# Kernel tuning notes

Hardware: AMD Instinct MI355X
Metric: run time of the kernel (lower is better)

## Reference

```python
import jax, jax.numpy as jnp
import numpy as np

D, H, F, L, V = 768, 4, 1024, 3, 10000
B, TLAB, S = 16, 513, 197
SCALE = 0.02


def setup_inputs() -> dict:
    key = jax.random.key(0)
    ks = jax.random.split(key, 16)
    inp = {
        'labels': jax.random.randint(ks[0], (B, TLAB), 0, V),
        'vision_feats': jax.random.normal(ks[1], (B, S, D), jnp.float32),
        'vis_proj_w': jax.random.normal(ks[2], (D, D), jnp.float32) * SCALE,
        'vis_proj_b': jnp.zeros((D,), jnp.float32),
        'tok_emb': jax.random.normal(ks[3], (V, D), jnp.float32) * SCALE,
        'pos_emb': jax.random.normal(ks[4], (1, 512, D), jnp.float32) * SCALE,
        'sa_w': jax.random.normal(ks[5], (L, 3 * D, D), jnp.float32) * SCALE,
        'sa_b': jnp.zeros((L, 3 * D), jnp.float32),
        'sa_out_w': jax.random.normal(ks[6], (L, D, D), jnp.float32) * SCALE,
        'sa_out_b': jnp.zeros((L, D), jnp.float32),
        'ca_w': jax.random.normal(ks[7], (L, 3 * D, D), jnp.float32) * SCALE,
        'ca_b': jnp.zeros((L, 3 * D), jnp.float32),
        'ca_out_w': jax.random.normal(ks[8], (L, D, D), jnp.float32) * SCALE,
        'ca_out_b': jnp.zeros((L, D), jnp.float32),
        'ln1_g': jnp.ones((L, D), jnp.float32), 'ln1_b': jnp.zeros((L, D), jnp.float32),
        'ln2_g': jnp.ones((L, D), jnp.float32), 'ln2_b': jnp.zeros((L, D), jnp.float32),
        'ln3_g': jnp.ones((L, D), jnp.float32), 'ln3_b': jnp.zeros((L, D), jnp.float32),
        'ff1_w': jax.random.normal(ks[9], (L, F, D), jnp.float32) * SCALE,
        'ff1_b': jnp.zeros((L, F), jnp.float32),
        'ff2_w': jax.random.normal(ks[10], (L, D, F), jnp.float32) * SCALE,
        'ff2_b': jnp.zeros((L, D), jnp.float32),
        'out_w': jax.random.normal(ks[11], (V, D), jnp.float32) * SCALE,
        'out_b': jnp.zeros((V,), jnp.float32),
    }
    return inp


def layer_norm(x, g, b, eps=1e-5):
    m = jnp.mean(x, axis=-1, keepdims=True)
    v = jnp.var(x, axis=-1, keepdims=True)
    return (x - m) / jnp.sqrt(v + eps) * g + b


def mha(qx, kx, vx, w, b, ow, ob, mask):
    # torch nn.MultiheadAttention with packed in_proj [3D, D]
    d = qx.shape[-1]
    hd = d // H
    q = qx @ w[:d].T + b[:d]
    k = kx @ w[d:2 * d].T + b[d:2 * d]
    v = vx @ w[2 * d:].T + b[2 * d:]
    def split(t):
        return t.reshape(t.shape[0], t.shape[1], H, hd).transpose(0, 2, 1, 3)
    q, k, v = split(q), split(k), split(v)  # [B,H,T,hd]
    s = jnp.einsum('bhqd,bhkd->bhqk', q, k) / jnp.sqrt(jnp.asarray(hd, qx.dtype))
    if mask is not None:
        s = s + mask
    a = jax.nn.softmax(s, axis=-1)
    o = jnp.einsum('bhqk,bhkd->bhqd', a, v)
    o = o.transpose(0, 2, 1, 3).reshape(qx.shape[0], qx.shape[1], d)
    return o @ ow.T + ob


def decode(labels, vision_feats, vis_proj_w, vis_proj_b, tok_emb, pos_emb,
           sa_w, sa_b, sa_out_w, sa_out_b, ca_w, ca_b, ca_out_w, ca_out_b,
           ln1_g, ln1_b, ln2_g, ln2_b, ln3_g, ln3_b,
           ff1_w, ff1_b, ff2_w, ff2_b, out_w, out_b):
    mem = vision_feats @ vis_proj_w.T + vis_proj_b          # [B,S,D]
    tgt_tok = labels[:, :-1]                                # [B,T] T=512
    T = tgt_tok.shape[1]
    x = tok_emb[tgt_tok] + pos_emb[:, :T, :]                # [B,T,D]
    # causal additive mask (teacher-forced loop == single full causal pass)
    mask = jnp.where(jnp.tril(jnp.ones((T, T), bool)), 0.0, -jnp.inf).astype(x.dtype)
    for l in range(L):
        x = layer_norm(x + mha(x, x, x, sa_w[l], sa_b[l], sa_out_w[l], sa_out_b[l], mask), ln1_g[l], ln1_b[l])
        x = layer_norm(x + mha(x, mem, mem, ca_w[l], ca_b[l], ca_out_w[l], ca_out_b[l], None), ln2_g[l], ln2_b[l])
        ff = jax.nn.relu(x @ ff1_w[l].T + ff1_b[l]) @ ff2_w[l].T + ff2_b[l]
        x = layer_norm(x + ff, ln3_g[l], ln3_b[l])
    return x @ out_w.T + out_b                              # [B,T,V]


def reference(labels, vision_feats, vis_proj_w, vis_proj_b, tok_emb, pos_emb,
              sa_w, sa_b, sa_out_w, sa_out_b, ca_w, ca_b, ca_out_w, ca_out_b,
              ln1_g, ln1_b, ln2_g, ln2_b, ln3_g, ln3_b,
              ff1_w, ff1_b, ff2_w, ff2_b, out_w, out_b):
    logits = decode(labels, vision_feats, vis_proj_w, vis_proj_b, tok_emb, pos_emb,
                    sa_w, sa_b, sa_out_w, sa_out_b, ca_w, ca_b, ca_out_w, ca_out_b,
                    ln1_g, ln1_b, ln2_g, ln2_b, ln3_g, ln3_b,
                    ff1_w, ff1_b, ff2_w, ff2_b, out_w, out_b)
    return (logits, labels[:, 1:])
```

## Files before the change

### kernel.cpp

```cpp
#include <hip/hip_runtime.h>
#include <hip/hip_fp8.h>

typedef unsigned short u16;
typedef float f32x4 __attribute__((ext_vector_type(4)));
typedef unsigned short u16x8 __attribute__((ext_vector_type(8)));
typedef unsigned short u16x4 __attribute__((ext_vector_type(4)));
typedef long i64;

typedef __attribute__((address_space(3))) unsigned char lds_u8_t;
typedef __attribute__((address_space(1))) const unsigned char glb_u8_t;

__device__ __forceinline__ u16 f2bf(float f) {
    union { float f; unsigned u; } v; v.f = f;
    unsigned r = v.u + 0x7FFFu + ((v.u >> 16) & 1u);
    return (u16)(r >> 16);
}
__device__ __forceinline__ float bf2f(u16 h) {
    union { unsigned u; float f; } v; v.u = ((unsigned)h) << 16; return v.f;
}
__device__ __forceinline__ unsigned char f2e4m3(float f) {
    __hip_fp8_e4m3 h(f);
    return (unsigned char)h.__x;
}

struct CastQ { const float* s[9]; unsigned char* d[9]; long n4[9]; float mul[9]; };
__global__ __launch_bounds__(256) void castq_kernel(CastQ a) {
    int seg = blockIdx.z;
    const float* s = a.s[seg];
    unsigned char* d = a.d[seg];
    long n4 = a.n4[seg];
    float mul = a.mul[seg];
    long i = (long)blockIdx.x * 256 + threadIdx.x;
    long stride = (long)gridDim.x * 256;
    for (; i < n4; i += stride) {
        float4 f = reinterpret_cast<const float4*>(s)[i];
        uchar4 o;
        o.x = f2e4m3(f.x * mul); o.y = f2e4m3(f.y * mul);
        o.z = f2e4m3(f.z * mul); o.w = f2e4m3(f.w * mul);
        reinterpret_cast<uchar4*>(d)[i] = o;
    }
}

__global__ __launch_bounds__(256) void embed_kernel(
    const int* __restrict__ labels, const float* __restrict__ tok_emb,
    const float* __restrict__ pos_emb, u16* __restrict__ xb,
    unsigned char* __restrict__ xq, float* __restrict__ lab_out)
{
    int wid = threadIdx.x >> 6, lane = threadIdx.x & 63;
    int r = blockIdx.x * 4 + wid;
    int b = r >> 9, t = r & 511;
    int tok = labels[b * 513 + t];
    if (lane == 0) lab_out[r] = (float)labels[b * 513 + t + 1];
    const float* te = tok_emb + (long)tok * 768;
    const float* pe = pos_emb + (long)t * 768;
    u16* xo = xb + (long)r * 768;
    unsigned char* qo = xq + (long)r * 768;
    int base = lane * 12;
#pragma unroll
    for (int c = 0; c < 3; c++) {
        float4 a = *reinterpret_cast<const float4*>(te + base + c * 4);
        float4 p = *reinterpret_cast<const float4*>(pe + base + c * 4);
        float v0 = a.x + p.x, v1 = a.y + p.y, v2 = a.z + p.z, v3 = a.w + p.w;
        ushort4 o; o.x = f2bf(v0); o.y = f2bf(v1); o.z = f2bf(v2); o.w = f2bf(v3);
        *reinterpret_cast<ushort4*>(xo + base + c * 4) = o;
        uchar4 q; q.x = f2e4m3(v0); q.y = f2e4m3(v1); q.z = f2e4m3(v2); q.w = f2e4m3(v3);
        *reinterpret_cast<uchar4*>(qo + base + c * 4) = q;
    }
}

template<int OUT, int RELU, int BM, int QKV, int CMODE>
__global__ __launch_bounds__(256, 4) void gemm8(
    const unsigned char* __restrict__ A, int lda, long sAb, long sAh,
    const unsigned char* __restrict__ W, int ldw, long sWb, long sWh,
    const float* __restrict__ bias, float outscale,
    void* __restrict__ C, int ldc, long sCb, long sCh,
    unsigned char* __restrict__ vt8,
    int M, int N, int K, int NH)
{
    constexpr int NREP = (BM == 128) ? 4 : 2;
    constexpr int AHALF = (BM == 128) ? 4096 : 2048;
    __shared__ __align__(16) unsigned char As0[BM * 64];
    __shared__ __align__(16) unsigned char As1[BM * 64];
    __shared__ __align__(16) unsigned char Bs0[128 * 64];
    __shared__ __align__(16) unsigned char Bs1[128 * 64];

    int z = blockIdx.z, zb = z / NH, zh = z % NH;
    const unsigned char* Ap = A + (long)zb * sAb + (long)zh * sAh;
    const unsigned char* Wp = W + (long)zb * sWb + (long)zh * sWh;
    long coff = (long)zb * sCb + (long)zh * sCh;

    int gx = (int)gridDim.x, gy = (int)gridDim.y;
    int nwg = gx * gy;
    int orig = (int)(blockIdx.y * gridDim.x + blockIdx.x);
    int q = nwg >> 3, r = nwg & 7;
    int xcd = orig & 7, loc = orig >> 3;
    int wg = (xcd < r ? xcd * (q + 1) : r * (q + 1) + (xcd - r) * q) + loc;
    int full = 8 * gy;
    int nsc = (gx + 7) >> 3;
    int sc = wg / full; if (sc > nsc - 1) sc = nsc - 1;
    int rem = wg - sc * full;
    int wdt = gx - sc * 8; if (wdt > 8) wdt = 8;
    int by = rem / wdt, bx = sc * 8 + rem % wdt;

    int m0 = by * BM, n0 = bx * 128;

    if constexpr (CMODE == 1) { if (n0 > m0 + BM - 1) return; }
    int Keff = K;
    if constexpr (CMODE == 2) { Keff = min(K, m0 + BM); }

    int tid = threadIdx.x, wid = tid >> 6, lane = tid & 63;
    int wr = (BM == 128) ? (wid >> 1) * 64 : 0;
    int wc = (BM == 128) ? (wid & 1) * 64 : wid * 32;
    int fr = lane & 15, gk = (lane >> 4) * 8;

    int li0 = wid * 64 + lane;
    int rsW = li0 >> 1, csW = li0 & 1;
    int kcW = ((csW ^ (rsW >> 2)) & 1) << 4;
    long woff = (long)min(n0 + rsW, N - 1) * ldw + kcW;
    long aoff;
    if constexpr (BM == 128) {
        aoff = (long)min(m0 + rsW, M - 1) * lda + kcW;
    } else {
        int halfA = li0 >> 7;
        int rsA = (li0 >> 1) & 63, csA = li0 & 1;
        int kcA = ((csA ^ (rsA >> 2)) & 1) << 4;
        aoff = (long)min(m0 + rsA, M - 1) * lda + halfA * 32 + kcA;
    }
    char* a0base = (char*)As0 + wid * 1024;
    char* a1base = (char*)As1 + wid * 1024;
    char* b0base = (char*)Bs0 + wid * 1024;
    char* b1base = (char*)Bs1 + wid * 1024;

    f32x4 acc[4][NREP] = {};

    auto stage = [&](char* ab, char* bb, int kt) {
        int k0 = kt * 64;
        if constexpr (BM == 128) {
            __builtin_amdgcn_global_load_lds((glb_u8_t*)(Ap + aoff + k0), (lds_u8_t*)ab, 16, 0, 0);
            __builtin_amdgcn_global_load_lds((glb_u8_t*)(Ap + aoff + k0 + 32), (lds_u8_t*)(ab + 4096), 16, 0, 0);
        } else {
            __builtin_amdgcn_global_load_lds((glb_u8_t*)(Ap + aoff + k0), (lds_u8_t*)ab, 16, 0, 0);
        }
        __builtin_amdgcn_global_load_lds((glb_u8_t*)(Wp + woff + k0), (lds_u8_t*)bb, 16, 0, 0);
        __builtin_amdgcn_global_load_lds((glb_u8_t*)(Wp + woff + k0 + 32), (lds_u8_t*)(bb + 4096), 16, 0, 0);
    };
    int cg = gk >> 4, go = gk & 15;
    auto compute = [&](const unsigned char* as, const unsigned char* bs) {
        i64 af[4][2], bw[NREP][2];
#pragma unroll
        for (int m = 0; m < 4; m++) {
            int rr2 = wr + m * 16 + fr;
            int off = rr2 * 32 + (((cg ^ (rr2 >> 2)) & 1) << 4) + go;
            af[m][0] = *reinterpret_cast<const i64*>(as + off);
            af[m][1] = *reinterpret_cast<const i64*>(as + AHALF + off);
        }
#pragma unroll
        for (int n = 0; n < NREP; n++) {
            int rr2 = wc + n * 16 + fr;
            int off = rr2 * 32 + (((cg ^ (rr2 >> 2)) & 1) << 4) + go;
            bw[n][0] = *reinterpret_cast<const i64*>(bs + off);
            bw[n][1] = *reinterpret_cast<const i64*>(bs + 4096 + off);
        }
#pragma unroll
        for (int ks = 0; ks < 2; ks++)
#pragma unroll
            for (int m = 0; m < 4; m++)
#pragma unroll
                for (int n = 0; n < NREP; n++)
                    acc[m][n] = __builtin_amdgcn_mfma_f32_16x16x32_fp8_fp8(
                        af[m][ks], bw[n][ks], acc[m][n], 0, 0, 0);
    };

    int nt = Keff >> 6;
    stage(a0base, b0base, 0);
    __syncthreads();
    for (int t = 0; t < nt; t += 2) {
        if (t + 1 < nt) stage(a1base, b1base, t + 1);
        compute(As0, Bs0);
        __syncthreads();
        if (t + 1 < nt) {
            if (t + 2 < nt) stage(a0base, b0base, t + 2);
            compute(As1, Bs1);
            __syncthreads();
        }
    }

    int crow = (lane >> 4) * 4;
#pragma unroll
    for (int m = 0; m < 4; m++) {
#pragma unroll
        for (int n = 0; n < NREP; n++) {
            int col = n0 + wc + n * 16 + fr;
            if (col >= N) continue;
            float bv = bias ? bias[col] : 0.f;
            int rbase = m0 + wr + m * 16 + crow;
            float vv[4];
#pragma unroll
            for (int rr = 0; rr < 4; rr++) {
                float v = acc[m][n][rr] * outscale + bv;
                if (RELU) v = fmaxf(v, 0.f);
                vv[rr] = v;
            }
            if constexpr (QKV) {
                if (col < 1536) {
#pragma unroll
                    for (int rr = 0; rr < 4; rr++)
                        ((unsigned char*)C)[coff + (long)(rbase + rr) * ldc + col] = f2e4m3(vv[rr]);
                } else {
                    int tt = col - 1536;
                    int h = tt / 192, d = tt - h * 192;
                    int b = rbase >> 9, k0 = rbase & 511;
                    uchar4 o;
                    o.x = f2e4m3(vv[0]); o.y = f2e4m3(vv[1]);
                    o.z = f2e4m3(vv[2]); o.w = f2e4m3(vv[3]);
                    *reinterpret_cast<uchar4*>(vt8 + ((long)((b << 2) + h) * 192 + d) * 512 + k0) = o;
                }
            } else {
#pragma unroll
                for (int rr = 0; rr < 4; rr++) {
                    int row = rbase + rr;
                    if (row >= M) continue;
                    long idx = coff + (long)row * ldc + col;
                    if (OUT == 0)      ((float*)C)[idx] = vv[rr];
                    else if (OUT == 1) ((u16*)C)[idx] = f2bf(vv[rr]);
                    else               ((unsigned char*)C)[idx] = f2e4m3(vv[rr]);
                }
            }
        }
    }
}

__global__ __launch_bounds__(256) void transpose_pad8(
    const unsigned char* __restrict__ V, long sVb, long sVh, int ldv, int NH,
    unsigned char* __restrict__ VT, long sVT, int rowsIn, int Kp)
{
    __shared__ unsigned char tile[32][33];
    int z = blockIdx.z, zb = z / NH, zh = z % NH;
    const unsigned char* Vp = V + (long)zb * sVb + (long)zh * sVh;
    int k0 = blockIdx.x * 32, d0 = blockIdx.y * 32;
#pragma unroll
    for (int i = 0; i < 4; i++) {
        int k = k0 + threadIdx.y + i * 8;
        int d = d0 + threadIdx.x;
        tile[threadIdx.y + i * 8][threadIdx.x] = (k < rowsIn) ? Vp[(long)k * ldv + d] : (unsigned char)0;
    }
    __syncthreads();
    unsigned char* Op = VT + (long)z * sVT;
#pragma unroll
    for (int i = 0; i < 4; i++) {
        int d = d0 + threadIdx.y + i * 8;
        int k = k0 + threadIdx.x;
        Op[(long)d * Kp + k] = tile[threadIdx.x][threadIdx.y + i * 8];
    }
}

template<int CPL, int CAUSAL>
__global__ __launch_bounds__(256) void softmax2(
    const u16* __restrict__ S, unsigned char* __restrict__ P,
    int ld_in, int valid_in, int ld_out, float scale)
{
    int wid = threadIdx.x >> 6, lane = threadIdx.x & 63;
    long r = (long)blockIdx.x * 4 + wid;
    int q = (int)(r & 511);
    int valid = CAUSAL ? (q + 1) : valid_in;
    const u16* srow = S + r * (long)ld_in;
    unsigned char* prow = P + r * (long)ld_out;
    int base = lane * CPL;
    float v[CPL];
    if constexpr (CPL == 8) {
        u16x8 x = *reinterpret_cast<const u16x8*>(srow + base);
#pragma unroll
        for (int j = 0; j < 8; j++) v[j] = bf2f(x[j]);
    } else {
        u16x4 x = *reinterpret_cast<const u16x4*>(srow + base);
#pragma unroll
        for (int j = 0; j < 4; j++) v[j] = bf2f(x[j]);
    }
    float mx = -3e38f;
#pragma unroll
    for (int j = 0; j < CPL; j++) {
        v[j] *= scale;
        if (base + j < valid) mx = fmaxf(mx, v[j]);
    }
#pragma unroll
    for (int o = 32; o; o >>= 1) mx = fmaxf(mx, __shfl_xor(mx, o, 64));
    float e[CPL], s = 0.f;
#pragma unroll
    for (int j = 0; j < CPL; j++) {
        e[j] = (base + j < valid) ? __expf(v[j] - mx) : 0.f;
        s += e[j];
    }
#pragma unroll
    for (int o = 32; o; o >>= 1) s += __shfl_xor(s, o, 64);
    float inv = 64.f / s;
    if constexpr (CPL == 8) {
        union { unsigned char b[8]; i64 v8; } o;
#pragma unroll
        for (int j = 0; j < 8; j++) o.b[j] = f2e4m3(e[j] * inv);
        *reinterpret_cast<i64*>(prow + base) = o.v8;
    } else {
        uchar4 o4;
        o4.x = f2e4m3(e[0] * inv); o4.y = f2e4m3(e[1] * inv);
        o4.z = f2e4m3(e[2] * inv); o4.w = f2e4m3(e[3] * inv);
        *reinterpret_cast<uchar4*>(prow + base) = o4;
    }
}

__global__ __launch_bounds__(256) void ln_kernel(
    const u16* __restrict__ xin, const u16* __restrict__ subb,
    const float* __restrict__ g, const float* __restrict__ bta,
    u16* __restrict__ xout, unsigned char* __restrict__ q8)
{
    int wid = threadIdx.x >> 6, lane = threadIdx.x & 63;
    long r = (long)blockIdx.x * 4 + wid;
    const u16* a = xin + r * 768;
    const u16* s = subb + r * 768;
    int base = lane * 12;
    float v[12];
    float sum = 0.f;
#pragma unroll
    for (int c = 0; c < 3; c++) {
        ushort4 av = *reinterpret_cast<const ushort4*>(a + base + c * 4);
        ushort4 sv = *reinterpret_cast<const ushort4*>(s + base + c * 4);
        v[c*4+0] = bf2f(av.x) + bf2f(sv.x);
        v[c*4+1] = bf2f(av.y) + bf2f(sv.y);
        v[c*4+2] = bf2f(av.z) + bf2f(sv.z);
        v[c*4+3] = bf2f(av.w) + bf2f(sv.w);
        sum += v[c*4+0] + v[c*4+1] + v[c*4+2] + v[c*4+3];
    }
#pragma unroll
    for (int o = 32; o; o >>= 1) sum += __shfl_xor(sum, o, 64);
    float mean = sum * (1.f / 768.f);
    float vs = 0.f;
#pragma unroll
    for (int j = 0; j < 12; j++) { float t = v[j] - mean; vs += t * t; }
#pragma unroll
    for (int o = 32; o; o >>= 1) vs += __shfl_xor(vs, o, 64);
    float rstd = rsqrtf(vs * (1.f / 768.f) + 1e-5f);
    u16* xo = xout + r * 768;
    unsigned char* qo = q8 + r * 768;
#pragma unroll
    for (int c = 0; c < 3; c++) {
        float4 gv = *reinterpret_cast<const float4*>(g + base + c * 4);
        float4 bv = *reinterpret_cast<const float4*>(bta + base + c * 4);
        float y0 = (v[c*4+0] - mean) * rstd * gv.x + bv.x;
        float y1 = (v[c*4+1] - mean) * rstd * gv.y + bv.y;
        float y2 = (v[c*4+2] - mean) * rstd * gv.z + bv.z;
        float y3 = (v[c*4+3] - mean) * rstd * gv.w + bv.w;
        ushort4 o; o.x = f2bf(y0); o.y = f2bf(y1); o.z = f2bf(y2); o.w = f2bf(y3);
        *reinterpret_cast<ushort4*>(xo + base + c * 4) = o;
        uchar4 qb; qb.x = f2e4m3(y0); qb.y = f2e4m3(y1); qb.z = f2e4m3(y2); qb.w = f2e4m3(y3);
        *reinterpret_cast<uchar4*>(qo + base + c * 4) = qb;
    }
}

template<int OUT, int RELU, int BM>
static void g8(hipStream_t st, const unsigned char* A, int lda, const unsigned char* W, int ldw,
               const float* bias, void* C, int ldc, int M, int N, int K) {
    dim3 g((N + 127) / 128, (M + BM - 1) / BM, 1), b(256, 1, 1);
    gemm8<OUT,RELU,BM,0,0><<<g,b,0,st>>>(A,lda,0,0,W,ldw,0,0,bias,1.f/256.f,C,ldc,0,0,nullptr,M,N,K,1);
}
template<int OUT, int CMODE>
static void g8bat(hipStream_t st,
    const unsigned char* A, int lda, long sAb, long sAh,
    const unsigned char* W, int ldw, long sWb, long sWh,
    float outscale, void* C, int ldc, long sCb, long sCh,
    int M, int N, int K, int Z, int NH) {
    dim3 g((N + 127) / 128, (M + 127) / 128, Z), b(256, 1, 1);
    gemm8<OUT,0,128,0,CMODE><<<g,b,0,st>>>(A,lda,sAb,sAh,W,ldw,sWb,sWh,nullptr,outscale,
                                           C,ldc,sCb,sCh,nullptr,M,N,K,NH);
}
static void g8qkv(hipStream_t st, const unsigned char* A, const unsigned char* W,
                  const float* bias, unsigned char* q8k8, unsigned char* vt8) {
    dim3 g(18, 64, 1), b(256, 1, 1);
    gemm8<2,0,128,1,0><<<g,b,0,st>>>(A,768,0,0,W,768,0,0,bias,1.f/256.f,
                                     q8k8,1536,0,0,vt8,8192,2304,768,1);
}

extern "C" void kernel_launch(void* const* d_in, const int* in_sizes, int n_in,
                              void* d_out, int out_size, void* d_ws, size_t ws_size,
                              hipStream_t stream)
{
    const int*   labels = (const int*)  d_in[0];
    const float* vision = (const float*)d_in[1];
    const float* vpw    = (const float*)d_in[2];
    const float* vpb    = (const float*)d_in[3];
    const float* temb   = (const float*)d_in[4];
    const float* pemb   = (const float*)d_in[5];
    const float* saw    = (const float*)d_in[6];
    const float* sab    = (const float*)d_in[7];
    const float* saow   = (const float*)d_in[8];
    const float* saob   = (const float*)d_in[9];
    const float* caw    = (const float*)d_in[10];
    const float* cab    = (const float*)d_in[11];
    const float* caow   = (const float*)d_in[12];
    const float* caob   = (const float*)d_in[13];
    const float* ln1g   = (const float*)d_in[14];
    const float* ln1b   = (const float*)d_in[15];
    const float* ln2g   = (const float*)d_in[16];
    const float* ln2b   = (const float*)d_in[17];
    const float* ln3g   = (const float*)d_in[18];
    const float* ln3b   = (const float*)d_in[19];
    const float* f1w    = (const float*)d_in[20];
    const float* f1b    = (const float*)d_in[21];
    const float* f2w    = (const float*)d_in[22];
    const float* f2b    = (const float*)d_in[23];
    const float* ow     = (const float*)d_in[24];
    const float* ob     = (const float*)d_in[25];
    (void)in_sizes; (void)n_in; (void)out_size;

    char* p = (char*)d_ws;
    auto alloc = [&](long elems, int esz) -> char* {
        char* r = p; p += ((long)elems * esz + 255) & ~255L; return r;
    };
    unsigned char* w8_sa  = (unsigned char*)alloc(3L*2304*768, 1);
    unsigned char* w8_ca  = (unsigned char*)alloc(3L*2304*768, 1);
    unsigned char* w8_sao = (unsigned char*)alloc(3L*768*768, 1);
    unsigned char* w8_cao = (unsigned char*)alloc(3L*768*768, 1);
    unsigned char* w8_f1  = (unsigned char*)alloc(3L*1024*768, 1);
    unsigned char* w8_f2  = (unsigned char*)alloc(3L*768*1024, 1);
    unsigned char* w8_ow  = (unsigned char*)alloc(10000L*768, 1);
    unsigned char* w8_vp  = (unsigned char*)alloc(768L*768, 1);
    unsigned char* vis8   = (unsigned char*)alloc(3152L*768, 1);
    unsigned char* mem8   = (unsigned char*)alloc(3152L*768, 1);
    unsigned char* xq     = (unsigned char*)alloc(8192L*768, 1);
    unsigned char* h8     = (unsigned char*)alloc(8192L*1024, 1);
    unsigned char* attn8  = (unsigned char*)alloc(8192L*768, 1);
    unsigned char* q8k8   = (unsigned char*)alloc(8192L*1536, 1);
    unsigned char* q8ca   = (unsigned char*)alloc(8192L*768, 1);
    unsigned char* kv8    = (unsigned char*)alloc(3152L*1536, 1);
    unsigned char* vt8    = (unsigned char*)alloc(64L*192*512, 1);
    unsigned char* pr8    = (unsigned char*)alloc(64L*512*512, 1);
    u16* xb   = (u16*)alloc(8192L*768, 2);
    u16* scb  = (u16*)alloc(64L*512*512, 2);
    u16* subb = (u16*)alloc(8192L*768, 2);
    if ((size_t)(p - (char*)d_ws) > ws_size) return;

    CastQ cq;
    cq.s[0] = saw;    cq.d[0] = w8_sa;  cq.n4[0] = 3L*2304*768/4;  cq.mul[0] = 256.f;
    cq.s[1] = caw;    cq.d[1] = w8_ca;  cq.n4[1] = 3L*2304*768/4;  cq.mul[1] = 256.f;
    cq.s[2] = saow;   cq.d[2] = w8_sao; cq.n4[2] = 3L*768*768/4;   cq.mul[2] = 256.f;
    cq.s[3] = caow;   cq.d[3] = w8_cao; cq.n4[3] = 3L*768*768/4;   cq.mul[3] = 256.f;
    cq.s[4] = f1w;    cq.d[4] = w8_f1;  cq.n4[4] = 3L*1024*768/4;  cq.mul[4] = 256.f;
    cq.s[5] = f2w;    cq.d[5] = w8_f2;  cq.n4[5] = 3L*768*1024/4;  cq.mul[5] = 256.f;
    cq.s[6] = ow;     cq.d[6] = w8_ow;  cq.n4[6] = 10000L*768/4;   cq.mul[6] = 256.f;
    cq.s[7] = vpw;    cq.d[7] = w8_vp;  cq.n4[7] = 768L*768/4;     cq.mul[7] = 256.f;
    cq.s[8] = vision; cq.d[8] = vis8;   cq.n4[8] = 3152L*768/4;    cq.mul[8] = 1.f;
    castq_kernel<<<dim3(512, 1, 9), dim3(256), 0, stream>>>(cq);

    embed_kernel<<<dim3(2048), dim3(256), 0, stream>>>(labels, temb, pemb, xb, xq,
                                                       (float*)d_out + 81920000L);

    g8<2,0,64>(stream, vis8, 768, w8_vp, 768, vpb, mem8, 768, 3152, 768, 768);

    const float scale = 0.07216878364870323f;
    const float PSCALE_INV = 1.f / 64.f;

    for (int l = 0; l < 3; l++) {
        g8qkv(stream, xq, w8_sa + (long)l*2304*768, sab + l*2304, q8k8, vt8);
        g8bat<1,1>(stream, q8k8, 1536, 512L*1536, 192, q8k8 + 768, 1536, 512L*1536, 192,
                   1.f, scb, 512, 4L*512*512, 512L*512, 512, 512, 192, 64, 4);
        softmax2<8,1><<<dim3(8192), dim3(256), 0, stream>>>(scb, pr8, 512, 512, 512, scale);
        g8bat<2,2>(stream, pr8, 512, 4L*512*512, 512L*512, vt8, 512, 4L*192*512, 192L*512,
                   PSCALE_INV, attn8, 768, 512L*768, 192, 512, 192, 512, 64, 4);
        g8<1,0,64>(stream, attn8, 768, w8_sao + (long)l*768*768, 768,
                   saob + l*768, subb, 768, 8192, 768, 768);
        ln_kernel<<<dim3(2048), dim3(256), 0, stream>>>(xb, subb, ln1g + l*768, ln1b + l*768,
                                                        xb, xq);

        g8<2,0,64>(stream, xq, 768, w8_ca + (long)l*2304*768, 768,
                   cab + l*2304, q8ca, 768, 8192, 768, 768);
        g8<2,0,64>(stream, mem8, 768, w8_ca + (long)l*2304*768 + 768L*768, 768,
                   cab + l*2304 + 768, kv8, 1536, 3152, 1536, 768);
        transpose_pad8<<<dim3(8,6,64), dim3(32,8), 0, stream>>>(
            kv8 + 768, 197L*1536, 192L, 1536, 4, vt8, 192L*256, 197, 256);
        g8bat<1,0>(stream, q8ca, 768, 512L*768, 192, kv8, 1536, 197L*1536, 192,
                   1.f, scb, 224, 4L*512*224, 512L*224, 512, 197, 192, 64, 4);
        softmax2<4,0><<<dim3(8192), dim3(256), 0, stream>>>(scb, pr8, 224, 197, 256, scale);
        g8bat<2,0>(stream, pr8, 256, 4L*512*256, 512L*256, vt8, 256, 4L*192*256, 192L*256,
                   PSCALE_INV, attn8, 768, 512L*768, 192, 512, 192, 256, 64, 4);
        g8<1,0,64>(stream, attn8, 768, w8_cao + (long)l*768*768, 768,
                   caob + l*768, subb, 768, 8192, 768, 768);
        ln_kernel<<<dim3(2048), dim3(256), 0, stream>>>(xb, subb, ln2g + l*768, ln2b + l*768,
                                                        xb, xq);

        g8<2,1,128>(stream, xq, 768, w8_f1 + (long)l*1024*768, 768, f1b + l*1024,
                    h8, 1024, 8192, 1024, 768);
        g8<1,0,64>(stream, h8, 1024, w8_f2 + (long)l*768*1024, 1024, f2b + l*768,
                   subb, 768, 8192, 768, 1024);
        ln_kernel<<<dim3(2048), dim3(256), 0, stream>>>(xb, subb, ln3g + l*768, ln3b + l*768,
                                                        xb, xq);
    }

    g8<0,0,128>(stream, xq, 768, w8_ow, 768, ob, (float*)d_out, 10000, 8192, 10000, 768);
}
```

Measured before the change: 1.068 ms.

## Fuse QK^T score GEMM with softmax into a single attention-probability kernel

Replaces the separate QK^T batched GEMM (bf16 score buffer) and row softmax kernels with one kernel that computes 128-row score tiles with FP8 MFMA, keeps per-tile exponentials as FP8 in LDS, and then rescales them using the combined row max and sum before writing FP8 probabilities. This removes the bf16 score round trip through global memory and one launch per attention. In exchange the kernel uses a large LDS footprint (about 115 KB), which limits occupancy, and launches only 256 workgroups. The probabilities are also quantized twice (per tile, then after rescaling), which adds some precision loss. The causal early-exit in the GEMM template is removed along with the old path.

Measured after the change: 1.185 ms. 1.11x slower.

```diff
diff --git a/kernel.cpp b/kernel.cpp
--- a/kernel.cpp
+++ b/kernel.cpp
@@ -21,6 +21,12 @@
 __device__ __forceinline__ unsigned char f2e4m3(float f) {
     __hip_fp8_e4m3 h(f);
     return (unsigned char)h.__x;
+}
+__device__ __forceinline__ float e4m32f(unsigned char b) {
+    int e = (b >> 3) & 15, m = b & 7;
+    union { unsigned u; float f; } p;
+    p.u = (unsigned)(e ? e + 117 : 118) << 23;
+    return (e ? (8 + m) : m) * p.f;
 }
 
 struct CastQ { const float* s[9]; unsigned char* d[9]; long n4[9]; float mul[9]; };
@@ -103,8 +109,6 @@
     int by = rem / wdt, bx = sc * 8 + rem % wdt;
 
     int m0 = by * BM, n0 = bx * 128;
-
-    if constexpr (CMODE == 1) { if (n0 > m0 + BM - 1) return; }
     int Keff = K;
     if constexpr (CMODE == 2) { Keff = min(K, m0 + BM); }
 
@@ -230,6 +234,179 @@
     }
 }
 
+template<int CAUSAL, int CPL>
+__global__ __launch_bounds__(256) void fused_sm(
+    const unsigned char* __restrict__ Q, int ldq, long sQb, long sQh,
+    const unsigned char* __restrict__ Kin, int ldk, long sKb, long sKh,
+    int krows,
+    unsigned char* __restrict__ P, int ldp, long sPz,
+    float scale)
+{
+    __shared__ __align__(16) unsigned char Qs[6 * 4096];
+    __shared__ __align__(16) unsigned char Ks[6 * 4096];
+    __shared__ __align__(16) unsigned char Sl[4 * 16384];
+    __shared__ float mt[4][128];
+    __shared__ float rsL[4][128];
+    __shared__ float tmpm[2][128], tmps[2][128];
+
+    int tid = threadIdx.x, wid = tid >> 6, lane = tid & 63;
+    int wr = (wid >> 1) * 64, wc = (wid & 1) * 64;
+    int fl = lane & 15, g = lane >> 4;
+    int cg = g >> 1, go = (g & 1) * 8;
+    int y = blockIdx.y, z = blockIdx.z, zb = z >> 2, zh = z & 3;
+    const unsigned char* Qp = Q + (long)zb * sQb + (long)zh * sQh;
+    const unsigned char* Kp2 = Kin + (long)zb * sKb + (long)zh * sKh;
+    int KT = CAUSAL ? (y + 1) : (CPL / 2);
+
+    int srow = tid >> 1, scs = tid & 1;
+    int skc = ((scs ^ (srow >> 2)) & 1) << 4;
+
+    {
+        const unsigned char* qb = Qp + (long)(y * 128 + srow) * ldq + skc;
+#pragma unroll
+        for (int hh = 0; hh < 6; hh++)
+            __builtin_amdgcn_global_load_lds((glb_u8_t*)(qb + hh * 32),
+                (lds_u8_t*)(Qs + hh * 4096 + wid * 1024), 16, 0, 0);
+        const unsigned char* kb = Kp2 + (long)min(srow, krows - 1) * ldk + skc;
+#pragma unroll
+        for (int hh = 0; hh < 6; hh++)
+            __builtin_amdgcn_global_load_lds((glb_u8_t*)(kb + hh * 32),
+                (lds_u8_t*)(Ks + hh * 4096 + wid * 1024), 16, 0, 0);
+    }
+    __syncthreads();
+
+    for (int kt = 0; kt < KT; ++kt) {
+        f32x4 acc[4][4] = {};
+#pragma unroll
+        for (int t = 0; t < 3; ++t) {
+            i64 af[4][2], bw[4][2];
+#pragma unroll
+            for (int m = 0; m < 4; m++) {
+                int rr2 = wr + m * 16 + fl;
+                int off = rr2 * 32 + (((cg ^ (rr2 >> 2)) & 1) << 4) + go;
+                af[m][0] = *reinterpret_cast<const i64*>(Qs + (2 * t) * 4096 + off);
+                af[m][1] = *reinterpret_cast<const i64*>(Qs + (2 * t + 1) * 4096 + off);
+            }
+#pragma unroll
+            for (int n = 0; n < 4; n++) {
+                int rr2 = wc + n * 16 + fl;
+                int off = rr2 * 32 + (((cg ^ (rr2 >> 2)) & 1) << 4) + go;
+                bw[n][0] = *reinterpret_cast<const i64*>(Ks + (2 * t) * 4096 + off);
+                bw[n][1] = *reinterpret_cast<const i64*>(Ks + (2 * t + 1) * 4096 + off);
+            }
+#pragma unroll
+            for (int ks = 0; ks < 2; ks++)
+#pragma unroll
+                for (int m = 0; m < 4; m++)
+#pragma unroll
+                    for (int n = 0; n < 4; n++)
+                        acc[m][n] = __builtin_amdgcn_mfma_f32_16x16x32_fp8_fp8(
+                            af[m][ks], bw[n][ks], acc[m][n], 0, 0, 0);
+        }
+        float rmx[4][4];
+#pragma unroll
+        for (int m = 0; m < 4; m++)
+#pragma unroll
+        for (int rr = 0; rr < 4; rr++) {
+            int rl = wr + m * 16 + g * 4 + rr;
+            int rowg = y * 128 + rl;
+            float mx = -3e38f;
+#pragma unroll
+            for (int n = 0; n < 4; n++) {
+                int col = kt * 128 + wc + n * 16 + fl;
+                bool ok = CAUSAL ? (col <= rowg) : (col < krows);
+                if (ok) mx = fmaxf(mx, acc[m][n][rr]);
+            }
+            mx = fmaxf(mx, __shfl_xor(mx, 1, 64));
+            mx = fmaxf(mx, __shfl_xor(mx, 2, 64));
+            mx = fmaxf(mx, __shfl_xor(mx, 4, 64));
+            mx = fmaxf(mx, __shfl_xor(mx, 8, 64));
+            rmx[m][rr] = mx;
+            if (fl == 0) tmpm[wid & 1][rl] = mx;
+        }
+        __syncthreads();
+        if (kt + 1 < KT) {
+            const unsigned char* kb = Kp2 + (long)min((kt + 1) * 128 + srow, krows - 1) * ldk + skc;
+#pragma unroll
+            for (int hh = 0; hh < 6; hh++)
+                __builtin_amdgcn_global_load_lds((glb_u8_t*)(kb + hh * 32),
+                    (lds_u8_t*)(Ks + hh * 4096 + wid * 1024), 16, 0, 0);
+        }
+#pragma unroll
+        for (int m = 0; m < 4; m++)
+#pragma unroll
+        for (int rr = 0; rr < 4; rr++) {
+            int rl = wr + m * 16 + g * 4 + rr;
+            float cm = fmaxf(tmpm[0][rl], tmpm[1][rl]);
+            rmx[m][rr] = cm;
+            if (fl == 0 && (wid & 1) == 0) mt[kt][rl] = cm;
+        }
+#pragma unroll
+        for (int m = 0; m < 4; m++)
+#pragma unroll
+        for (int rr = 0; rr < 4; rr++) {
+            int rl = wr + m * 16 + g * 4 + rr;
+            int rowg = y * 128 + rl;
+            int swz = ((rl >> 2) & 3) << 4;
+            float sum = 0.f;
+#pragma unroll
+            for (int n = 0; n < 4; n++) {
+                int ct = wc + n * 16 + fl;
+                int col = kt * 128 + ct;
+                bool ok = CAUSAL ? (col <= rowg) : (col < krows);
+                float pv = ok ? __expf((acc[m][n][rr] - rmx[m][rr]) * scale) : 0.f;
+                sum += pv;
+                Sl[kt * 16384 + rl * 128 + (ct ^ swz)] = f2e4m3(pv);
+            }
+            sum += __shfl_xor(sum, 1, 64);
+            sum += __shfl_xor(sum, 2, 64);
+            sum += __shfl_xor(sum, 4, 64);
+            sum += __shfl_xor(sum, 8, 64);
+            if (fl == 0) tmps[wid & 1][rl] = sum;
+        }
+        __syncthreads();
+#pragma unroll
+        for (int m = 0; m < 4; m++)
+#pragma unroll
+        for (int rr = 0; rr < 4; rr++) {
+            int rl = wr + m * 16 + g * 4 + rr;
+            if (fl == 0 && (wid & 1) == 0) rsL[kt][rl] = tmps[0][rl] + tmps[1][rl];
+        }
+    }
+    __syncthreads();
+
+    for (int r8 = 0; r8 < 32; ++r8) {
+        int rl = wid * 32 + r8;
+        float mf = -3e38f;
+        for (int kt = 0; kt < KT; ++kt) mf = fmaxf(mf, mt[kt][rl]);
+        float l = 0.f;
+        for (int kt = 0; kt < KT; ++kt) l += rsL[kt][rl] * __expf((mt[kt][rl] - mf) * scale);
+        int cw0 = lane * CPL;
+        int tile = cw0 >> 7;
+        if (tile < KT) {
+            float ft = __expf((mt[tile][rl] - mf) * scale) * 64.f / l;
+            int swz = ((rl >> 2) & 3) << 4;
+            const unsigned char* src = Sl + tile * 16384 + rl * 128 + ((cw0 & 127) ^ swz);
+            unsigned char* dst = P + (long)z * sPz + (long)(y * 128 + rl) * ldp + cw0;
+            if constexpr (CPL == 8) {
+                i64 v8 = *reinterpret_cast<const i64*>(src);
+                const unsigned char* bp = reinterpret_cast<const unsigned char*>(&v8);
+                union { unsigned char b[8]; i64 v; } o;
+#pragma unroll
+                for (int j = 0; j < 8; j++) o.b[j] = f2e4m3(e4m32f(bp[j]) * ft);
+                *reinterpret_cast<i64*>(dst) = o.v;
+            } else {
+                unsigned v4 = *reinterpret_cast<const unsigned*>(src);
+                const unsigned char* bp = reinterpret_cast<const unsigned char*>(&v4);
+                union { unsigned char b[4]; unsigned v; } o;
+#pragma unroll
+                for (int j = 0; j < 4; j++) o.b[j] = f2e4m3(e4m32f(bp[j]) * ft);
+                *reinterpret_cast<unsigned*>(dst) = o.v;
+            }
+        }
+    }
+}
+
 __global__ __launch_bounds__(256) void transpose_pad8(
     const unsigned char* __restrict__ V, long sVb, long sVh, int ldv, int NH,
     unsigned char* __restrict__ VT, long sVT, int rowsIn, int Kp)
@@ -251,58 +428,6 @@
         int d = d0 + threadIdx.y + i * 8;
         int k = k0 + threadIdx.x;
         Op[(long)d * Kp + k] = tile[threadIdx.x][threadIdx.y + i * 8];
-    }
-}
-
-template<int CPL, int CAUSAL>
-__global__ __launch_bounds__(256) void softmax2(
-    const u16* __restrict__ S, unsigned char* __restrict__ P,
-    int ld_in, int valid_in, int ld_out, float scale)
-{
-    int wid = threadIdx.x >> 6, lane = threadIdx.x & 63;
-    long r = (long)blockIdx.x * 4 + wid;
-    int q = (int)(r & 511);
-    int valid = CAUSAL ? (q + 1) : valid_in;
-    const u16* srow = S + r * (long)ld_in;
-    unsigned char* prow = P + r * (long)ld_out;
-    int base = lane * CPL;
-    float v[CPL];
-    if constexpr (CPL == 8) {
-        u16x8 x = *reinterpret_cast<const u16x8*>(srow + base);
-#pragma unroll
-        for (int j = 0; j < 8; j++) v[j] = bf2f(x[j]);
-    } else {
-        u16x4 x = *reinterpret_cast<const u16x4*>(srow + base);
-#pragma unroll
-        for (int j = 0; j < 4; j++) v[j] = bf2f(x[j]);
-    }
-    float mx = -3e38f;
-#pragma unroll
-    for (int j = 0; j < CPL; j++) {
-        v[j] *= scale;
-        if (base + j < valid) mx = fmaxf(mx, v[j]);
-    }
-#pragma unroll
-    for (int o = 32; o; o >>= 1) mx = fmaxf(mx, __shfl_xor(mx, o, 64));
-    float e[CPL], s = 0.f;
-#pragma unroll
-    for (int j = 0; j < CPL; j++) {
-        e[j] = (base + j < valid) ? __expf(v[j] - mx) : 0.f;
-        s += e[j];
-    }
-#pragma unroll
-    for (int o = 32; o; o >>= 1) s += __shfl_xor(s, o, 64);
-    float inv = 64.f / s;
-    if constexpr (CPL == 8) {
-        union { unsigned char b[8]; i64 v8; } o;
-#pragma unroll
-        for (int j = 0; j < 8; j++) o.b[j] = f2e4m3(e[j] * inv);
-        *reinterpret_cast<i64*>(prow + base) = o.v8;
-    } else {
-        uchar4 o4;
-        o4.x = f2e4m3(e[0] * inv); o4.y = f2e4m3(e[1] * inv);
-        o4.z = f2e4m3(e[2] * inv); o4.w = f2e4m3(e[3] * inv);
-        *reinterpret_cast<uchar4*>(prow + base) = o4;
     }
 }
 
@@ -432,7 +557,6 @@
     unsigned char* vt8    = (unsigned char*)alloc(64L*192*512, 1);
     unsigned char* pr8    = (unsigned char*)alloc(64L*512*512, 1);
     u16* xb   = (u16*)alloc(8192L*768, 2);
-    u16* scb  = (u16*)alloc(64L*512*512, 2);
     u16* subb = (u16*)alloc(8192L*768, 2);
     if ((size_t)(p - (char*)d_ws) > ws_size) return;
 
@@ -458,9 +582,9 @@
 
     for (int l = 0; l < 3; l++) {
         g8qkv(stream, xq, w8_sa + (long)l*2304*768, sab + l*2304, q8k8, vt8);
-        g8bat<1,1>(stream, q8k8, 1536, 512L*1536, 192, q8k8 + 768, 1536, 512L*1536, 192,
-                   1.f, scb, 512, 4L*512*512, 512L*512, 512, 512, 192, 64, 4);
-        softmax2<8,1><<<dim3(8192), dim3(256), 0, stream>>>(scb, pr8, 512, 512, 512, scale);
+        fused_sm<1,8><<<dim3(1,4,64), dim3(256), 0, stream>>>(
+            q8k8, 1536, 512L*1536, 192, q8k8 + 768, 1536, 512L*1536, 192,
+            512, pr8, 512, 512L*512, scale);
         g8bat<2,2>(stream, pr8, 512, 4L*512*512, 512L*512, vt8, 512, 4L*192*512, 192L*512,
                    PSCALE_INV, attn8, 768, 512L*768, 192, 512, 192, 512, 64, 4);
         g8<1,0,64>(stream, attn8, 768, w8_sao + (long)l*768*768, 768,
@@ -474,9 +598,9 @@
                    cab + l*2304 + 768, kv8, 1536, 3152, 1536, 768);
         transpose_pad8<<<dim3(8,6,64), dim3(32,8), 0, stream>>>(
             kv8 + 768, 197L*1536, 192L, 1536, 4, vt8, 192L*256, 197, 256);
-        g8bat<1,0>(stream, q8ca, 768, 512L*768, 192, kv8, 1536, 197L*1536, 192,
-                   1.f, scb, 224, 4L*512*224, 512L*224, 512, 197, 192, 64, 4);
-        softmax2<4,0><<<dim3(8192), dim3(256), 0, stream>>>(scb, pr8, 224, 197, 256, scale);
+        fused_sm<0,4><<<dim3(1,4,64), dim3(256), 0, stream>>>(
+            q8ca, 768, 512L*768, 192, kv8, 1536, 197L*1536, 192,
+            197, pr8, 256, 512L*256, scale);
         g8bat<2,0>(stream, pr8, 256, 4L*512*256, 512L*256, vt8, 256, 4L*192*256, 192L*256,
                    PSCALE_INV, attn8, 768, 512L*768, 192, 512, 192, 256, 64, 4);
         g8<1,0,64>(stream, attn8, 768, w8_cao + (long)l*768*768, 768,
```
